# Optimization experiments

Measured on AMD Instinct MI355X. Metric: run time of the kernel, lower is better.

## Reference

```python
import jax, jax.numpy as jnp
import numpy as np

N_SRC = 100000
E = 300000
D = 256
HEADS = 8
D_K = D // HEADS
N_EXPERTS = 5


def setup_inputs() -> dict:
    key = jax.random.key(0)
    kx, ki, ke, kw, kb = jax.random.split(key, 5)
    x = jax.random.normal(kx, (N_SRC, D), dtype=jnp.float32)
    index = jax.random.randint(ki, (E,), 0, N_SRC)
    # disjoint routing masks: each output row handled by exactly one of 5 linears
    expert_id = jax.random.randint(ke, (E,), 0, N_EXPERTS)
    masks = expert_id[None, :] == jnp.arange(N_EXPERTS)[:, None]  # [5, E] bool
    # learned params: 5 independent Linear(D, D) layers (torch layout: y = x @ W.T + b)
    bound = 1.0 / np.sqrt(D)
    W = jax.random.uniform(kw, (N_EXPERTS, D, D), minval=-bound, maxval=bound, dtype=jnp.float32)
    b = jax.random.uniform(kb, (N_EXPERTS, D), minval=-bound, maxval=bound, dtype=jnp.float32)
    return {"x": x, "W": W, "b": b, "index": index, "masks": masks}


def reference(x, W, b, index, masks):
    # gather source rows for every output slot: [E, D]
    xi = x[index]
    out = jnp.zeros((xi.shape[0], D), dtype=x.dtype)
    # sequential masked overwrite matches torch's output[mask] = ... semantics
    for i in range(N_EXPERTS):
        yi = xi @ W[i].T + b[i]  # [E, D]
        out = jnp.where(masks[i][:, None], yi, out)
    return out.reshape(xi.shape[0], HEADS, D_K)
```

## Files before the change

### kernel.cpp

```cpp
#include <hip/hip_runtime.h>

#define E_TOT   300000
#define D_DIM   256
#define N_EXP   5
#define BM      64
#define LDK     264
#define LDF     260
#define NB_CNT  ((E_TOT + 255) / 256)
#define MAX_TILES (E_TOT / BM + N_EXP)

typedef __attribute__((ext_vector_type(8))) short bf16x8;
typedef __attribute__((ext_vector_type(4))) float f32x4;

__device__ inline unsigned short f2bf(float f) {
  union { float f; unsigned u; } v; v.f = f;
  unsigned u = v.u;
  u += 0x7FFFu + ((u >> 16) & 1u);
  return (unsigned short)(u >> 16);
}

__device__ inline int get_expert(const void* masks, int e, bool is_u8) {
  if (is_u8) {
    const unsigned char* m = (const unsigned char*)masks;
#pragma unroll
    for (int i = 0; i < N_EXP; ++i) if (m[(size_t)i * E_TOT + e]) return i;
  } else {
    const int* m = (const int*)masks;
#pragma unroll
    for (int i = 0; i < N_EXP; ++i) if (m[(size_t)i * E_TOT + e]) return i;
  }
  return 0;
}

__global__ void prep_kernel(const float* __restrict__ W, unsigned short* __restrict__ Wbf,
                            const void* __restrict__ masks, int* __restrict__ hdr,
                            int doConv) {
  __shared__ int wc[4][N_EXP];
  __shared__ int s_u8ok;
  const int tt = threadIdx.x, w = tt >> 6, lane = tt & 63;
  const int gtid = (int)blockIdx.x * 256 + tt;

  const unsigned char* m8 = (const unsigned char*)masks;
  int cnt1 = 1, ex = -1;
  if (gtid < E_TOT) {
    cnt1 = 0; int exu = 0;
#pragma unroll
    for (int i = 0; i < N_EXP; ++i) {
      int tb = (m8[(size_t)i * E_TOT + gtid] != 0);
      cnt1 += tb; if (tb) exu = i;
    }
    ex = exu;
  }
  if (tt == 0) s_u8ok = 1;
  __syncthreads();
  if (cnt1 != 1) s_u8ok = 0;
  __syncthreads();
  const int is_u8 = s_u8ok;
  if (!is_u8 && gtid < E_TOT) ex = get_expert(masks, gtid, false);

#pragma unroll
  for (int i = 0; i < N_EXP; ++i) {
    unsigned long long bal = __ballot(ex == i);
    if (lane == 0) wc[w][i] = __popcll(bal);
  }
  if (doConv) {
    const int n4 = (N_EXP * D_DIM * D_DIM) / 4;
    for (int i = gtid; i < n4; i += (int)gridDim.x * 256) {
      float4 v = ((const float4*)W)[i];
      ushort4 o4;
      o4.x = f2bf(v.x); o4.y = f2bf(v.y); o4.z = f2bf(v.z); o4.w = f2bf(v.w);
      ((ushort4*)Wbf)[i] = o4;
    }
  }
  __syncthreads();
  if (tt < N_EXP)
    atomicAdd(&hdr[tt], wc[0][tt] + wc[1][tt] + wc[2][tt] + wc[3][tt]);
  if (tt == 0 && blockIdx.x == 0) hdr[6] = is_u8;
}

__global__ void scatter_kernel(const void* __restrict__ masks, const int* __restrict__ hdr,
                               int* __restrict__ cursor, int* __restrict__ perm) {
  __shared__ int wc[4][N_EXP];
  __shared__ int wo[4][N_EXP];
  __shared__ int bb[N_EXP];
  const int tt = threadIdx.x, w = tt >> 6, lane = tt & 63;
  const int e = (int)blockIdx.x * 256 + tt;
  const bool is_u8 = (hdr[6] != 0);

  int ex = (e < E_TOT) ? get_expert(masks, e, is_u8) : -1;
  unsigned long long myBal = 0;
#pragma unroll
  for (int i = 0; i < N_EXP; ++i) {
    unsigned long long bal = __ballot(ex == i);
    if (lane == 0) wc[w][i] = __popcll(bal);
    if (ex == i) myBal = bal;
  }
  __syncthreads();
  if (tt < 4 * N_EXP) {
    int ww = tt / N_EXP, ii = tt % N_EXP;
    int s = 0;
    for (int p = 0; p < ww; ++p) s += wc[p][ii];
    wo[ww][ii] = s;
  }
  if (tt < N_EXP) {
    int tot = wc[0][tt] + wc[1][tt] + wc[2][tt] + wc[3][tt];
    int old = atomicAdd(&cursor[tt], tot);
    int base = 0;
    for (int i = 0; i < tt; ++i) base += hdr[i];
    bb[tt] = base + old;
  }
  __syncthreads();
  if (ex >= 0) {
    int rank = __popcll(myBal & ((1ull << lane) - 1ull));
    perm[bb[ex] + wo[w][ex] + rank] = e;
  }
}

template <bool PRE>
__launch_bounds__(256, 4)
__global__ void gemm_kernel(const float* __restrict__ x, const float* __restrict__ W,
                            const unsigned short* __restrict__ Wbf,
                            const float* __restrict__ bias, const int* __restrict__ index,
                            const int* __restrict__ hdr, const int* __restrict__ perm,
                            float* __restrict__ out) {
  __shared__ __align__(16) unsigned short lA[BM * LDK];
  __shared__ int srcRow[BM];
  __shared__ int outRow[BM];

  int t = (int)blockIdx.x;
  int ex = -1, trow = 0, cnt = 0, accT = 0, base = 0, run = 0;
#pragma unroll
  for (int i = 0; i < N_EXP; ++i) {
    int c = hdr[i];
    int nt = (c + BM - 1) / BM;
    if (ex < 0 && t < accT + nt) { ex = i; trow = t - accT; cnt = c; base = run; }
    accT += nt;
    run += c;
  }
  if (ex < 0) return;
  int row0 = base + trow * BM;
  int rows = min(BM, cnt - trow * BM);

  const int tt = threadIdx.x;
  if (tt < BM) {
    int rr = min(tt, rows - 1);
    int e = perm[row0 + rr];
    outRow[tt] = e;
    srcRow[tt] = index[e];
  }
  __syncthreads();

#pragma unroll
  for (int i = 0; i < 16; ++i) {
    int lin = i * 256 + tt;
    int rr = lin >> 6;
    int c4 = lin & 63;
    const float4 v = ((const float4*)(x + (size_t)srcRow[rr] * D_DIM))[c4];
    ushort4 o4;
    o4.x = f2bf(v.x); o4.y = f2bf(v.y); o4.z = f2bf(v.z); o4.w = f2bf(v.w);
    *(ushort4*)&lA[rr * LDK + c4 * 4] = o4;
  }
  __syncthreads();

  const int w = tt >> 6, lane = tt & 63, quad = lane >> 4, l16 = lane & 15;

  f32x4 acc[4][4];
#pragma unroll
  for (int mt = 0; mt < 4; ++mt)
#pragma unroll
    for (int nt = 0; nt < 4; ++nt) acc[mt][nt] = (f32x4){0.f, 0.f, 0.f, 0.f};

#pragma unroll
  for (int ks = 0; ks < 8; ++ks) {
    int k0 = ks * 32 + quad * 8;
    bf16x8 a[4], b[4];
#pragma unroll
    for (int mt = 0; mt < 4; ++mt)
      a[mt] = *(const bf16x8*)&lA[(mt * 16 + l16) * LDK + k0];
#pragma unroll
    for (int nt = 0; nt < 4; ++nt) {
      int col = w * 64 + nt * 16 + l16;
      if (PRE) {
        b[nt] = *(const bf16x8*)&Wbf[((size_t)ex * D_DIM + col) * D_DIM + k0];
      } else {
        const float* wp = W + ((size_t)ex * D_DIM + col) * D_DIM + k0;
        float4 v0 = ((const float4*)wp)[0];
        float4 v1 = ((const float4*)wp)[1];
        bf16x8 bb;
        bb[0] = (short)f2bf(v0.x); bb[1] = (short)f2bf(v0.y);
        bb[2] = (short)f2bf(v0.z); bb[3] = (short)f2bf(v0.w);
        bb[4] = (short)f2bf(v1.x); bb[5] = (short)f2bf(v1.y);
        bb[6] = (short)f2bf(v1.z); bb[7] = (short)f2bf(v1.w);
        b[nt] = bb;
      }
    }
#pragma unroll
    for (int mt = 0; mt < 4; ++mt)
#pragma unroll
      for (int nt = 0; nt < 4; ++nt)
        acc[mt][nt] = __builtin_amdgcn_mfma_f32_16x16x32_bf16(a[mt], b[nt], acc[mt][nt], 0, 0, 0);
  }

  float bv[4];
#pragma unroll
  for (int nt = 0; nt < 4; ++nt) bv[nt] = bias[ex * D_DIM + w * 64 + nt * 16 + l16];

  float* lsf = (float*)lA;
#pragma unroll
  for (int chunk = 0; chunk < 2; ++chunk) {
    __syncthreads();
#pragma unroll
    for (int mtl = 0; mtl < 2; ++mtl) {
      int mt = chunk * 2 + mtl;
#pragma unroll
      for (int nt = 0; nt < 4; ++nt) {
        int col = w * 64 + nt * 16 + l16;
#pragma unroll
        for (int r = 0; r < 4; ++r) {
          int lr = mtl * 16 + quad * 4 + r;
          lsf[lr * LDF + col] = acc[mt][nt][r] + bv[nt];
        }
      }
    }
    __syncthreads();
    int r8 = tt >> 3, c8 = tt & 7;
    int grow = chunk * 32 + r8;
    if (grow < rows) {
      float* op = out + (size_t)outRow[grow] * D_DIM;
#pragma unroll
      for (int j = 0; j < 8; ++j) {
        int c4 = c8 + j * 8;
        f32x4 v4 = *(const f32x4*)&lsf[r8 * LDF + c4 * 4];
        __builtin_nontemporal_store(v4, (f32x4*)(op + c4 * 4));
      }
    }
  }
}

extern "C" void kernel_launch(void* const* d_in, const int* in_sizes, int n_in,
                              void* d_out, int out_size, void* d_ws, size_t ws_size,
                              hipStream_t stream) {
  const float* x     = (const float*)d_in[0];
  const float* W     = (const float*)d_in[1];
  const float* bias  = (const float*)d_in[2];
  const int*   index = (const int*)d_in[3];
  const void*  masks = d_in[4];
  float* out = (float*)d_out;

  int* hdr = (int*)d_ws;
  const size_t wbfB  = (size_t)N_EXP * D_DIM * D_DIM * 2;
  const size_t permB = (size_t)E_TOT * 4;
  bool pre = (ws_size >= 1024 + wbfB + permB);
  size_t off = 1024;
  unsigned short* Wbf = nullptr;
  if (pre) { Wbf = (unsigned short*)((char*)d_ws + off); off += wbfB; }
  int* perm = (int*)((char*)d_ws + off);

  (void)hipMemsetAsync(d_ws, 0, 1024, stream);
  prep_kernel<<<NB_CNT, 256, 0, stream>>>(W, Wbf, masks, hdr, pre ? 1 : 0);
  scatter_kernel<<<NB_CNT, 256, 0, stream>>>(masks, hdr, hdr + 16, perm);
  if (pre)
    gemm_kernel<true><<<MAX_TILES, 256, 0, stream>>>(x, W, Wbf, bias, index, hdr, perm, out);
  else
    gemm_kernel<false><<<MAX_TILES, 256, 0, stream>>>(x, W, Wbf, bias, index, hdr, perm, out);
}
```

Before: 478.5 us.

## Merge count and scatter passes using fixed per-expert perm segments

When the workspace is large enough, each expert gets its own fixed-size segment of the permutation buffer at offset expert*E. This removes the need for a prior global count pass, so the counting, weight conversion and scatter run in one kernel, and the GEMM reads the final cursors as counts. It saves a kernel launch and a second read of the masks, at the cost of a workspace five times larger for perm.

Measured after the change: 463.4 us. 1.03x faster.

```diff
diff --git a/kernel.cpp b/kernel.cpp
--- a/kernel.cpp
+++ b/kernel.cpp
@@ -32,6 +32,70 @@
   return 0;
 }
 
+__global__ void scatter_conv_kernel(const float* __restrict__ W,
+                                    unsigned short* __restrict__ Wbf,
+                                    const void* __restrict__ masks,
+                                    int* __restrict__ cursor, int* __restrict__ perm,
+                                    int doConv) {
+  __shared__ int wc[4][N_EXP];
+  __shared__ int wo[4][N_EXP];
+  __shared__ int bb[N_EXP];
+  __shared__ int s_u8ok;
+  const int tt = threadIdx.x, w = tt >> 6, lane = tt & 63;
+  const int e = (int)blockIdx.x * 256 + tt;
+
+  const unsigned char* m8 = (const unsigned char*)masks;
+  int cnt1 = 1, ex = -1;
+  if (e < E_TOT) {
+    cnt1 = 0; int exu = 0;
+#pragma unroll
+    for (int i = 0; i < N_EXP; ++i) {
+      int tb = (m8[(size_t)i * E_TOT + e] != 0);
+      cnt1 += tb; if (tb) exu = i;
+    }
+    ex = exu;
+  }
+  if (tt == 0) s_u8ok = 1;
+  __syncthreads();
+  if (cnt1 != 1) s_u8ok = 0;
+  __syncthreads();
+  if (!s_u8ok && e < E_TOT) ex = get_expert(masks, e, false);
+
+  unsigned long long myBal = 0;
+#pragma unroll
+  for (int i = 0; i < N_EXP; ++i) {
+    unsigned long long bal = __ballot(ex == i);
+    if (lane == 0) wc[w][i] = __popcll(bal);
+    if (ex == i) myBal = bal;
+  }
+  if (doConv) {
+    const int n4 = (N_EXP * D_DIM * D_DIM) / 4;
+    for (int i = e; i < n4; i += (int)gridDim.x * 256) {
+      float4 v = ((const float4*)W)[i];
+      ushort4 o4;
+      o4.x = f2bf(v.x); o4.y = f2bf(v.y); o4.z = f2bf(v.z); o4.w = f2bf(v.w);
+      ((ushort4*)Wbf)[i] = o4;
+    }
+  }
+  __syncthreads();
+  if (tt < 4 * N_EXP) {
+    int ww = tt / N_EXP, ii = tt % N_EXP;
+    int s = 0;
+    for (int p = 0; p < ww; ++p) s += wc[p][ii];
+    wo[ww][ii] = s;
+  }
+  if (tt < N_EXP) {
+    int tot = wc[0][tt] + wc[1][tt] + wc[2][tt] + wc[3][tt];
+    int old = atomicAdd(&cursor[tt], tot);
+    bb[tt] = tt * E_TOT + old;
+  }
+  __syncthreads();
+  if (ex >= 0) {
+    int rank = __popcll(myBal & ((1ull << lane) - 1ull));
+    perm[bb[ex] + wo[w][ex] + rank] = e;
+  }
+}
+
 __global__ void prep_kernel(const float* __restrict__ W, unsigned short* __restrict__ Wbf,
                             const void* __restrict__ masks, int* __restrict__ hdr,
                             int doConv) {
@@ -116,12 +180,12 @@
   }
 }
 
-template <bool PRE>
+template <bool PRE, bool FIXB>
 __launch_bounds__(256, 4)
 __global__ void gemm_kernel(const float* __restrict__ x, const float* __restrict__ W,
                             const unsigned short* __restrict__ Wbf,
                             const float* __restrict__ bias, const int* __restrict__ index,
-                            const int* __restrict__ hdr, const int* __restrict__ perm,
+                            const int* __restrict__ cnts, const int* __restrict__ perm,
                             float* __restrict__ out) {
   __shared__ __align__(16) unsigned short lA[BM * LDK];
   __shared__ int srcRow[BM];
@@ -131,14 +195,14 @@
   int ex = -1, trow = 0, cnt = 0, accT = 0, base = 0, run = 0;
 #pragma unroll
   for (int i = 0; i < N_EXP; ++i) {
-    int c = hdr[i];
+    int c = cnts[i];
     int nt = (c + BM - 1) / BM;
     if (ex < 0 && t < accT + nt) { ex = i; trow = t - accT; cnt = c; base = run; }
     accT += nt;
     run += c;
   }
   if (ex < 0) return;
-  int row0 = base + trow * BM;
+  int row0 = (FIXB ? ex * E_TOT : base) + trow * BM;
   int rows = min(BM, cnt - trow * BM);
 
   const int tt = threadIdx.x;
@@ -250,17 +314,27 @@
   int* hdr = (int*)d_ws;
   const size_t wbfB  = (size_t)N_EXP * D_DIM * D_DIM * 2;
   const size_t permB = (size_t)E_TOT * 4;
-  bool pre = (ws_size >= 1024 + wbfB + permB);
+  const bool fix3 = (ws_size >= 1024 + wbfB + (size_t)N_EXP * permB);
+  const bool pre  = fix3 || (ws_size >= 1024 + wbfB + permB);
   size_t off = 1024;
   unsigned short* Wbf = nullptr;
   if (pre) { Wbf = (unsigned short*)((char*)d_ws + off); off += wbfB; }
   int* perm = (int*)((char*)d_ws + off);
 
   (void)hipMemsetAsync(d_ws, 0, 1024, stream);
-  prep_kernel<<<NB_CNT, 256, 0, stream>>>(W, Wbf, masks, hdr, pre ? 1 : 0);
-  scatter_kernel<<<NB_CNT, 256, 0, stream>>>(masks, hdr, hdr + 16, perm);
-  if (pre)
-    gemm_kernel<true><<<MAX_TILES, 256, 0, stream>>>(x, W, Wbf, bias, index, hdr, perm, out);
-  else
-    gemm_kernel<false><<<MAX_TILES, 256, 0, stream>>>(x, W, Wbf, bias, index, hdr, perm, out);
-}
+
+  if (fix3) {
+    scatter_conv_kernel<<<NB_CNT, 256, 0, stream>>>(W, Wbf, masks, hdr + 16, perm, 1);
+    gemm_kernel<true, true><<<MAX_TILES, 256, 0, stream>>>(x, W, Wbf, bias, index,
+                                                           hdr + 16, perm, out);
+  } else {
+    prep_kernel<<<NB_CNT, 256, 0, stream>>>(W, Wbf, masks, hdr, pre ? 1 : 0);
+    scatter_kernel<<<NB_CNT, 256, 0, stream>>>(masks, hdr, hdr + 16, perm);
+    if (pre)
+      gemm_kernel<true, false><<<MAX_TILES, 256, 0, stream>>>(x, W, Wbf, bias, index,
+                                                              hdr, perm, out);
+    else
+      gemm_kernel<false, false><<<MAX_TILES, 256, 0, stream>>>(x, W, Wbf, bias, index,
+                                                               hdr, perm, out);
+  }
+}
```
